# Kernel tuning notes

Measured on AMD Instinct MI355X. Metric: run time of the kernel, lower is better.

The kernel has to match this reference:

```python
import jax, jax.numpy as jnp
import numpy as np

B, T, K = 1024, 512, 48
NEG = -10000.0
START, STOP = K - 2, K - 1


def setup_inputs() -> dict:
    key = jax.random.key(0)
    k1, k2, k3 = jax.random.split(key, 3)
    feats = jax.random.normal(k1, (B, T, K), dtype=jnp.float32)
    transitions = jax.random.normal(k2, (K, K), dtype=jnp.float32) * 0.1
    tags = jax.random.randint(k3, (B, T), 0, K - 2)
    return {"feats": feats, "transitions": transitions, "tags": tags}


def _mask_trans(transitions):
    # transitions[next, prev]; never transition INTO START, never OUT of STOP
    t = transitions.at[START, :].set(NEG)
    t = t.at[:, STOP].set(NEG)
    return t


def _forward_alg(feats, trans):
    # feats: [T, K] -> log partition (scalar)
    Kt = feats.shape[-1]
    init = jnp.full((Kt,), NEG, dtype=feats.dtype).at[START].set(0.0)

    def step(alpha, emit):
        # alpha[prev] + trans[next, prev] -> LSE over prev, add emit[next]
        alpha_new = emit + jax.nn.logsumexp(alpha[None, :] + trans, axis=1)
        return alpha_new, None

    alpha, _ = jax.lax.scan(step, init, feats)
    return jax.nn.logsumexp(alpha + trans[STOP])


def _gold_score(feats, trans, tags):
    # feats: [T, K], tags: [T]
    Tt = tags.shape[0]
    prev = jnp.concatenate([jnp.array([START], dtype=tags.dtype), tags[:-1]])
    emit = feats[jnp.arange(Tt), tags].sum()
    tr = trans[tags, prev].sum()
    return emit + tr + trans[STOP, tags[-1]]


def _viterbi(feats, trans):
    Kt = feats.shape[-1]
    init = jnp.full((Kt,), NEG, dtype=feats.dtype).at[START].set(0.0)

    def step(v, emit):
        scores = v[None, :] + trans           # [next, prev]
        bp = jnp.argmax(scores, axis=1)       # best prev for each next
        v_new = jnp.max(scores, axis=1) + emit
        return v_new, bp

    v, bps = jax.lax.scan(step, init, feats)  # bps: [T, K]
    term = v + trans[STOP]
    best_last = jnp.argmax(term)
    path_score = term[best_last]

    def back(tag, bp):
        return bp[tag], tag

    _, path = jax.lax.scan(back, best_last, bps, reverse=True)
    return path_score, path.astype(jnp.int32)


def reference(feats, transitions, tags):
    trans = _mask_trans(transitions)
    logZ = jax.vmap(lambda f: _forward_alg(f, trans))(feats)            # [B]
    gold = jax.vmap(lambda f, t: _gold_score(f, trans, t))(feats, tags)  # [B]
    nll = logZ - gold                                                    # [B]
    path_score, paths = jax.vmap(lambda f: _viterbi(f, trans))(feats)    # [B], [B,T]
    return nll, path_score, paths
```

## Files before the change

### kernel.cpp

```cpp
#include <hip/hip_runtime.h>
#include <math.h>

#define KS 48
#define TLEN 512
#define BN 1024
#define START_S 46
#define STOP_S 47
#define NEGV -10000.0f
#define PF 8

typedef float v2f __attribute__((ext_vector_type(2)));

__device__ __forceinline__ float bcast_lane0(float v) {
    return __builtin_bit_cast(float, __builtin_amdgcn_readfirstlane(__builtin_bit_cast(int, v)));
}

__device__ __forceinline__ void wargmax(float& bv, int& bi) {
    #pragma unroll
    for (int off = 32; off; off >>= 1) {
        float ov = __shfl_xor(bv, off, 64);
        int   oi = __shfl_xor(bi, off, 64);
        if (ov > bv || (ov == bv && oi < bi)) { bv = ov; bi = oi; }
    }
}

__global__ __launch_bounds__(64) void crf11(
    const float* __restrict__ feats,
    const float* __restrict__ trans,
    const int*   __restrict__ tags,
    float*       __restrict__ out,
    unsigned char* __restrict__ bp_g)
{
    const int lane = threadIdx.x;
    const bool act = lane < KS;

    __shared__ float xbuf[64];
    __shared__ __align__(16) unsigned char seg[64 * KS];
    __shared__ unsigned char path_sh[TLEN];

    if (blockIdx.x < BN) {
        const int b = blockIdx.x;
        const float* fb = feats + (size_t)b * TLEN * KS;
        const int*   tb = tags + (size_t)b * TLEN;

        float Erow[KS];
        {
            const float* tr = trans + (act ? lane : 0) * KS;
            #pragma unroll
            for (int p = 0; p < KS; ++p) {
                float tv = act ? tr[p] : NEGV;
                if (lane == START_S) tv = NEGV;
                if (p == STOP_S)     tv = NEGV;
                Erow[p] = __expf(tv);
            }
        }
        float tstart = act ? trans[lane * KS + START_S] : NEGV;
        if (lane == START_S) tstart = NEGV;

        float alpha = (act ? fb[lane] : -INFINITY) + tstart;

        auto fstep = [&](float emv) {
            float s  = bcast_lane0(alpha);
            float ue = __expf(alpha - s);
            xbuf[lane] = ue;
            const float4* uu = (const float4*)xbuf;
            v2f acc0 = {0.f, 0.f}, acc1 = {0.f, 0.f};
            #pragma unroll
            for (int g = 0; g < KS / 4; ++g) {
                float4 u = uu[g];
                v2f ua = {u.x, u.y}, ub = {u.z, u.w};
                v2f ea = {Erow[4 * g + 0], Erow[4 * g + 1]};
                v2f eb = {Erow[4 * g + 2], Erow[4 * g + 3]};
                acc0 = __builtin_elementwise_fma(ua, ea, acc0);
                acc1 = __builtin_elementwise_fma(ub, eb, acc1);
            }
            alpha = emv + s + __logf((acc0.x + acc0.y) + (acc1.x + acc1.y));
        };

        float em[PF];
        #pragma unroll
        for (int j = 0; j < PF; ++j)
            em[j] = act ? fb[(1 + j) * KS + lane] : -INFINITY;
        for (int c = 0; c < 63; ++c) {
            const int t0 = 1 + c * PF;
            float em_n[PF];
            #pragma unroll
            for (int j = 0; j < PF; ++j) {
                int tf = t0 + PF + j;
                em_n[j] = (act && tf < TLEN) ? fb[tf * KS + lane] : -INFINITY;
            }
            #pragma unroll
            for (int j = 0; j < PF; ++j) fstep(em[j]);
            #pragma unroll
            for (int j = 0; j < PF; ++j) em[j] = em_n[j];
        }
        #pragma unroll
        for (int j = 0; j < 7; ++j) fstep(em[j]);

        float tstop = act ? trans[STOP_S * KS + lane] : NEGV;
        if (lane == STOP_S) tstop = NEGV;
        float z = alpha + tstop;
        float mz = z;
        #pragma unroll
        for (int off = 32; off; off >>= 1)
            mz = fmaxf(mz, __shfl_xor(mz, off, 64));
        float se = __expf(z - mz);
        #pragma unroll
        for (int off = 32; off; off >>= 1)
            se += __shfl_xor(se, off, 64);
        float logZ = mz + __logf(se);

        float g = 0.0f;
        for (int t = lane; t < TLEN; t += 64) {
            int tg = tb[t];
            int pg = (t == 0) ? START_S : tb[t - 1];
            g += fb[t * KS + tg] + trans[tg * KS + pg];
        }
        #pragma unroll
        for (int off = 32; off; off >>= 1)
            g += __shfl_xor(g, off, 64);
        g += trans[STOP_S * KS + tb[TLEN - 1]];

        if (lane == 0) out[b] = logZ - g;
    } else {
        const int b = blockIdx.x - BN;
        const float* fb = feats + (size_t)b * TLEN * KS;
        unsigned char* bpb = bp_g + (size_t)b * TLEN * KS;

        float Trow[KS];
        {
            const float* tr = trans + (act ? lane : 0) * KS;
            #pragma unroll
            for (int p = 0; p < KS; ++p) {
                float tv = act ? tr[p] : NEGV;
                if (lane == START_S) tv = NEGV;
                if (p == STOP_S)     tv = NEGV;
                Trow[p] = tv;
            }
        }

        float vit = (lane == START_S) ? 0.0f : NEGV;

        auto vstep = [&](float emv, int t) {
            xbuf[lane] = vit;
            const float4* ww = (const float4*)xbuf;
            float bs[12]; int ib[12];
            #pragma unroll
            for (int g = 0; g < KS / 4; ++g) {
                float4 w = ww[g];
                v2f wa = {w.x, w.y}, wb = {w.z, w.w};
                v2f ta = {Trow[4 * g + 0], Trow[4 * g + 1]};
                v2f tc = {Trow[4 * g + 2], Trow[4 * g + 3]};
                v2f sa = wa + ta;
                v2f sb = wb + tc;
                float m01 = fmaxf(sa.x, sa.y); int i01 = (sa.y > sa.x) ? 4 * g + 1 : 4 * g + 0;
                float m23 = fmaxf(sb.x, sb.y); int i23 = (sb.y > sb.x) ? 4 * g + 3 : 4 * g + 2;
                bs[g] = fmaxf(m01, m23);       ib[g] = (m23 > m01) ? i23 : i01;
            }
            #pragma unroll
            for (int st = 0; st < 6; ++st) {
                float a = bs[2 * st], c2 = bs[2 * st + 1];
                int ia = ib[2 * st], ic = ib[2 * st + 1];
                bs[st] = fmaxf(a, c2); ib[st] = (c2 > a) ? ic : ia;
            }
            #pragma unroll
            for (int st = 0; st < 3; ++st) {
                float a = bs[2 * st], c2 = bs[2 * st + 1];
                int ia = ib[2 * st], ic = ib[2 * st + 1];
                bs[st] = fmaxf(a, c2); ib[st] = (c2 > a) ? ic : ia;
            }
            float best = fmaxf(bs[0], bs[1]);
            int   bi   = (bs[1] > bs[0]) ? ib[1] : ib[0];
            bi   = (bs[2] > best) ? ib[2] : bi;
            best = fmaxf(best, bs[2]);
            if (act) seg[(t & 63) * KS + lane] = (unsigned char)bi;
            vit = best + emv;
        };

        float em[PF];
        #pragma unroll
        for (int j = 0; j < PF; ++j)
            em[j] = act ? fb[j * KS + lane] : 0.0f;
        for (int c = 0; c < 64; ++c) {
            const int t0 = c * PF;
            float em_n[PF];
            if (c < 63) {
                #pragma unroll
                for (int j = 0; j < PF; ++j)
                    em_n[j] = act ? fb[(t0 + PF + j) * KS + lane] : 0.0f;
            }
            #pragma unroll
            for (int j = 0; j < PF; ++j) vstep(em[j], t0 + j);
            if ((c & 7) == 7 && c < 56) {
                const float4* s4 = (const float4*)seg;
                float4* d4 = (float4*)(bpb + (size_t)(c - 7) * PF * KS);
                #pragma unroll
                for (int i = 0; i < 3; ++i)
                    d4[lane + 64 * i] = s4[lane + 64 * i];
            }
            if (c < 63) {
                #pragma unroll
                for (int j = 0; j < PF; ++j) em[j] = em_n[j];
            }
        }

        asm volatile("s_waitcnt vmcnt(0)" ::: "memory");

        float tstop = act ? trans[STOP_S * KS + lane] : NEGV;
        if (lane == STOP_S) tstop = NEGV;
        float term = act ? (vit + tstop) : -3.0e38f;
        float bv = term;
        int   bidx = act ? lane : 9999;
        wargmax(bv, bidx);
        if (lane == 0) out[BN + b] = bv;

        int tag = bidx;
        for (int t = 63; t >= 0; --t) {
            path_sh[448 + t] = (unsigned char)tag;
            tag = seg[t * KS + tag];
        }
        for (int s = 6; s >= 0; --s) {
            float4 tmp[3];
            const float4* src = (const float4*)(bpb + (size_t)s * 64 * KS);
            #pragma unroll
            for (int i = 0; i < 3; ++i)
                tmp[i] = src[lane + 64 * i];
            float4* dst = (float4*)seg;
            #pragma unroll
            for (int i = 0; i < 3; ++i)
                dst[lane + 64 * i] = tmp[i];
            for (int t = 63; t >= 0; --t) {
                path_sh[s * 64 + t] = (unsigned char)tag;
                tag = seg[t * KS + tag];
            }
        }
        __syncthreads();
        float* pout = out + 2 * BN + (size_t)b * TLEN;
        for (int t = lane; t < TLEN; t += 64)
            pout[t] = (float)path_sh[t];
    }
}

extern "C" void kernel_launch(void* const* d_in, const int* in_sizes, int n_in,
                              void* d_out, int out_size, void* d_ws, size_t ws_size,
                              hipStream_t stream) {
    const float* feats = (const float*)d_in[0];
    const float* trans = (const float*)d_in[1];
    const int*   tags  = (const int*)d_in[2];
    float*       out   = (float*)d_out;
    (void)in_sizes; (void)n_in; (void)out_size; (void)ws_size;

    crf11<<<dim3(2 * BN), dim3(64), 0, stream>>>(feats, trans, tags, out,
                                                 (unsigned char*)d_ws);
}
```

Baseline: 441.5 us.

## Fuse forward-algorithm and Viterbi recursions into one wave per sequence

Replaces the split launch (separate blocks for logZ and Viterbi per sequence) with a single block per sequence that interleaves the Viterbi step and the forward step at each time position. Emissions are loaded from global memory once and shared by both recursions, and the two independent dependency chains give the scheduler ILP to hide latency. The backpointer staging buffer is doubled to 128 rows so the last segment stays in LDS. In exchange each wave holds both Trow and Erow in registers (higher VGPR use), and only 1024 waves are launched instead of 2048, which lowers occupancy and parallelism across the GPU.

```diff
diff --git a/kernel.cpp b/kernel.cpp
--- a/kernel.cpp
+++ b/kernel.cpp
@@ -24,7 +24,7 @@
     }
 }
 
-__global__ __launch_bounds__(64) void crf11(
+__global__ __launch_bounds__(64) void crf13(
     const float* __restrict__ feats,
     const float* __restrict__ trans,
     const int*   __restrict__ tags,
@@ -34,71 +34,130 @@
     const int lane = threadIdx.x;
     const bool act = lane < KS;
 
-    __shared__ float xbuf[64];
-    __shared__ __align__(16) unsigned char seg[64 * KS];
+    __shared__ float xf[64];
+    __shared__ float xv[64];
+    __shared__ __align__(16) unsigned char seg[128 * KS];
     __shared__ unsigned char path_sh[TLEN];
 
-    if (blockIdx.x < BN) {
-        const int b = blockIdx.x;
-        const float* fb = feats + (size_t)b * TLEN * KS;
-        const int*   tb = tags + (size_t)b * TLEN;
-
-        float Erow[KS];
-        {
-            const float* tr = trans + (act ? lane : 0) * KS;
+    const int b = blockIdx.x;
+    const float* fb = feats + (size_t)b * TLEN * KS;
+    const int*   tb = tags + (size_t)b * TLEN;
+    unsigned char* bpb = bp_g + (size_t)b * TLEN * KS;
+
+    float Erow[KS], Trow[KS];
+    {
+        const float* tr = trans + (act ? lane : 0) * KS;
+        #pragma unroll
+        for (int p = 0; p < KS; ++p) {
+            float tv = act ? tr[p] : NEGV;
+            if (lane == START_S) tv = NEGV;
+            if (p == STOP_S)     tv = NEGV;
+            Trow[p] = tv;
+            Erow[p] = __expf(tv);
+        }
+    }
+    float tstart = act ? trans[lane * KS + START_S] : NEGV;
+    if (lane == START_S) tstart = NEGV;
+
+    float alpha;
+    auto fstep = [&](float emv) {
+        float s  = bcast_lane0(alpha);
+        float ue = __expf(alpha - s);
+        xf[lane] = ue;
+        const float4* uu = (const float4*)xf;
+        v2f acc0 = {0.f, 0.f}, acc1 = {0.f, 0.f};
+        #pragma unroll
+        for (int g = 0; g < KS / 4; ++g) {
+            float4 u = uu[g];
+            v2f ua = {u.x, u.y}, ub = {u.z, u.w};
+            v2f ea = {Erow[4 * g + 0], Erow[4 * g + 1]};
+            v2f eb = {Erow[4 * g + 2], Erow[4 * g + 3]};
+            acc0 = __builtin_elementwise_fma(ua, ea, acc0);
+            acc1 = __builtin_elementwise_fma(ub, eb, acc1);
+        }
+        alpha = emv + s + __logf((acc0.x + acc0.y) + (acc1.x + acc1.y));
+    };
+
+    float vit = (lane == START_S) ? 0.0f : NEGV;
+    auto vstep = [&](float emv, int t) {
+        xv[lane] = vit;
+        const float4* ww = (const float4*)xv;
+        float bs[12]; int ib[12];
+        #pragma unroll
+        for (int g = 0; g < KS / 4; ++g) {
+            float4 w = ww[g];
+            v2f wa = {w.x, w.y}, wb = {w.z, w.w};
+            v2f ta = {Trow[4 * g + 0], Trow[4 * g + 1]};
+            v2f tc = {Trow[4 * g + 2], Trow[4 * g + 3]};
+            v2f sa = wa + ta;
+            v2f sb = wb + tc;
+            float m01 = fmaxf(sa.x, sa.y); int i01 = (sa.y > sa.x) ? 4 * g + 1 : 4 * g + 0;
+            float m23 = fmaxf(sb.x, sb.y); int i23 = (sb.y > sb.x) ? 4 * g + 3 : 4 * g + 2;
+            bs[g] = fmaxf(m01, m23);       ib[g] = (m23 > m01) ? i23 : i01;
+        }
+        #pragma unroll
+        for (int st = 0; st < 6; ++st) {
+            float a = bs[2 * st], c2 = bs[2 * st + 1];
+            int ia = ib[2 * st], ic = ib[2 * st + 1];
+            bs[st] = fmaxf(a, c2); ib[st] = (c2 > a) ? ic : ia;
+        }
+        #pragma unroll
+        for (int st = 0; st < 3; ++st) {
+            float a = bs[2 * st], c2 = bs[2 * st + 1];
+            int ia = ib[2 * st], ic = ib[2 * st + 1];
+            bs[st] = fmaxf(a, c2); ib[st] = (c2 > a) ? ic : ia;
+        }
+        float best = fmaxf(bs[0], bs[1]);
+        int   bi   = (bs[1] > bs[0]) ? ib[1] : ib[0];
+        bi   = (bs[2] > best) ? ib[2] : bi;
+        best = fmaxf(best, bs[2]);
+        if (act) seg[(t & 127) * KS + lane] = (unsigned char)bi;
+        vit = best + emv;
+    };
+
+    float r0 = act ? fb[lane] : 0.0f;
+    alpha = (act ? r0 : -INFINITY) + tstart;
+    vstep(r0, 0);
+
+    float em[PF];
+    #pragma unroll
+    for (int j = 0; j < PF; ++j)
+        em[j] = act ? fb[(1 + j) * KS + lane] : 0.0f;
+    for (int c = 0; c < 63; ++c) {
+        const int t0 = 1 + c * PF;
+        float em_n[PF];
+        #pragma unroll
+        for (int j = 0; j < PF; ++j) {
+            int tf = t0 + PF + j;
+            em_n[j] = (act && tf < TLEN) ? fb[tf * KS + lane] : 0.0f;
+        }
+        #pragma unroll
+        for (int j = 0; j < PF; ++j) {
+            vstep(em[j], t0 + j);
+            fstep(em[j]);
+        }
+        if ((c & 7) == 7 && c < 56) {
+            const int g = c >> 3;
+            const float4* s4 = (const float4*)(seg + (g & 1) * 64 * KS);
+            float4* d4 = (float4*)(bpb + (size_t)g * 64 * KS);
             #pragma unroll
-            for (int p = 0; p < KS; ++p) {
-                float tv = act ? tr[p] : NEGV;
-                if (lane == START_S) tv = NEGV;
-                if (p == STOP_S)     tv = NEGV;
-                Erow[p] = __expf(tv);
-            }
-        }
-        float tstart = act ? trans[lane * KS + START_S] : NEGV;
-        if (lane == START_S) tstart = NEGV;
-
-        float alpha = (act ? fb[lane] : -INFINITY) + tstart;
-
-        auto fstep = [&](float emv) {
-            float s  = bcast_lane0(alpha);
-            float ue = __expf(alpha - s);
-            xbuf[lane] = ue;
-            const float4* uu = (const float4*)xbuf;
-            v2f acc0 = {0.f, 0.f}, acc1 = {0.f, 0.f};
-            #pragma unroll
-            for (int g = 0; g < KS / 4; ++g) {
-                float4 u = uu[g];
-                v2f ua = {u.x, u.y}, ub = {u.z, u.w};
-                v2f ea = {Erow[4 * g + 0], Erow[4 * g + 1]};
-                v2f eb = {Erow[4 * g + 2], Erow[4 * g + 3]};
-                acc0 = __builtin_elementwise_fma(ua, ea, acc0);
-                acc1 = __builtin_elementwise_fma(ub, eb, acc1);
-            }
-            alpha = emv + s + __logf((acc0.x + acc0.y) + (acc1.x + acc1.y));
-        };
-
-        float em[PF];
-        #pragma unroll
-        for (int j = 0; j < PF; ++j)
-            em[j] = act ? fb[(1 + j) * KS + lane] : -INFINITY;
-        for (int c = 0; c < 63; ++c) {
-            const int t0 = 1 + c * PF;
-            float em_n[PF];
-            #pragma unroll
-            for (int j = 0; j < PF; ++j) {
-                int tf = t0 + PF + j;
-                em_n[j] = (act && tf < TLEN) ? fb[tf * KS + lane] : -INFINITY;
-            }
-            #pragma unroll
-            for (int j = 0; j < PF; ++j) fstep(em[j]);
-            #pragma unroll
-            for (int j = 0; j < PF; ++j) em[j] = em_n[j];
-        }
-        #pragma unroll
-        for (int j = 0; j < 7; ++j) fstep(em[j]);
-
-        float tstop = act ? trans[STOP_S * KS + lane] : NEGV;
-        if (lane == STOP_S) tstop = NEGV;
+            for (int i = 0; i < 3; ++i)
+                d4[lane + 64 * i] = s4[lane + 64 * i];
+        }
+        #pragma unroll
+        for (int j = 0; j < PF; ++j) em[j] = em_n[j];
+    }
+    #pragma unroll
+    for (int j = 0; j < 7; ++j) {
+        vstep(em[j], 505 + j);
+        fstep(em[j]);
+    }
+
+    asm volatile("s_waitcnt vmcnt(0)" ::: "memory");
+
+    float tstop = act ? trans[STOP_S * KS + lane] : NEGV;
+    if (lane == STOP_S) tstop = NEGV;
+    {
         float z = alpha + tstop;
         float mz = z;
         #pragma unroll
@@ -122,123 +181,38 @@
         g += trans[STOP_S * KS + tb[TLEN - 1]];
 
         if (lane == 0) out[b] = logZ - g;
-    } else {
-        const int b = blockIdx.x - BN;
-        const float* fb = feats + (size_t)b * TLEN * KS;
-        unsigned char* bpb = bp_g + (size_t)b * TLEN * KS;
-
-        float Trow[KS];
-        {
-            const float* tr = trans + (act ? lane : 0) * KS;
-            #pragma unroll
-            for (int p = 0; p < KS; ++p) {
-                float tv = act ? tr[p] : NEGV;
-                if (lane == START_S) tv = NEGV;
-                if (p == STOP_S)     tv = NEGV;
-                Trow[p] = tv;
-            }
-        }
-
-        float vit = (lane == START_S) ? 0.0f : NEGV;
-
-        auto vstep = [&](float emv, int t) {
-            xbuf[lane] = vit;
-            const float4* ww = (const float4*)xbuf;
-            float bs[12]; int ib[12];
-            #pragma unroll
-            for (int g = 0; g < KS / 4; ++g) {
-                float4 w = ww[g];
-                v2f wa = {w.x, w.y}, wb = {w.z, w.w};
-                v2f ta = {Trow[4 * g + 0], Trow[4 * g + 1]};
-                v2f tc = {Trow[4 * g + 2], Trow[4 * g + 3]};
-                v2f sa = wa + ta;
-                v2f sb = wb + tc;
-                float m01 = fmaxf(sa.x, sa.y); int i01 = (sa.y > sa.x) ? 4 * g + 1 : 4 * g + 0;
-                float m23 = fmaxf(sb.x, sb.y); int i23 = (sb.y > sb.x) ? 4 * g + 3 : 4 * g + 2;
-                bs[g] = fmaxf(m01, m23);       ib[g] = (m23 > m01) ? i23 : i01;
-            }
-            #pragma unroll
-            for (int st = 0; st < 6; ++st) {
-                float a = bs[2 * st], c2 = bs[2 * st + 1];
-                int ia = ib[2 * st], ic = ib[2 * st + 1];
-                bs[st] = fmaxf(a, c2); ib[st] = (c2 > a) ? ic : ia;
-            }
-            #pragma unroll
-            for (int st = 0; st < 3; ++st) {
-                float a = bs[2 * st], c2 = bs[2 * st + 1];
-                int ia = ib[2 * st], ic = ib[2 * st + 1];
-                bs[st] = fmaxf(a, c2); ib[st] = (c2 > a) ? ic : ia;
-            }
-            float best = fmaxf(bs[0], bs[1]);
-            int   bi   = (bs[1] > bs[0]) ? ib[1] : ib[0];
-            bi   = (bs[2] > best) ? ib[2] : bi;
-            best = fmaxf(best, bs[2]);
-            if (act) seg[(t & 63) * KS + lane] = (unsigned char)bi;
-            vit = best + emv;
-        };
-
-        float em[PF];
-        #pragma unroll
-        for (int j = 0; j < PF; ++j)
-            em[j] = act ? fb[j * KS + lane] : 0.0f;
-        for (int c = 0; c < 64; ++c) {
-            const int t0 = c * PF;
-            float em_n[PF];
-            if (c < 63) {
-                #pragma unroll
-                for (int j = 0; j < PF; ++j)
-                    em_n[j] = act ? fb[(t0 + PF + j) * KS + lane] : 0.0f;
-            }
-            #pragma unroll
-            for (int j = 0; j < PF; ++j) vstep(em[j], t0 + j);
-            if ((c & 7) == 7 && c < 56) {
-                const float4* s4 = (const float4*)seg;
-                float4* d4 = (float4*)(bpb + (size_t)(c - 7) * PF * KS);
-                #pragma unroll
-                for (int i = 0; i < 3; ++i)
-                    d4[lane + 64 * i] = s4[lane + 64 * i];
-            }
-            if (c < 63) {
-                #pragma unroll
-                for (int j = 0; j < PF; ++j) em[j] = em_n[j];
-            }
-        }
-
-        asm volatile("s_waitcnt vmcnt(0)" ::: "memory");
-
-        float tstop = act ? trans[STOP_S * KS + lane] : NEGV;
-        if (lane == STOP_S) tstop = NEGV;
-        float term = act ? (vit + tstop) : -3.0e38f;
-        float bv = term;
-        int   bidx = act ? lane : 9999;
-        wargmax(bv, bidx);
-        if (lane == 0) out[BN + b] = bv;
-
-        int tag = bidx;
+    }
+
+    float term = act ? (vit + tstop) : -3.0e38f;
+    float bv = term;
+    int   bidx = act ? lane : 9999;
+    wargmax(bv, bidx);
+    if (lane == 0) out[BN + b] = bv;
+
+    int tag = bidx;
+    for (int t = 63; t >= 0; --t) {
+        path_sh[448 + t] = (unsigned char)tag;
+        tag = seg[(64 + t) * KS + tag];
+    }
+    for (int s = 6; s >= 0; --s) {
+        float4 tmp[3];
+        const float4* src = (const float4*)(bpb + (size_t)s * 64 * KS);
+        #pragma unroll
+        for (int i = 0; i < 3; ++i)
+            tmp[i] = src[lane + 64 * i];
+        float4* dst = (float4*)seg;
+        #pragma unroll
+        for (int i = 0; i < 3; ++i)
+            dst[lane + 64 * i] = tmp[i];
         for (int t = 63; t >= 0; --t) {
-            path_sh[448 + t] = (unsigned char)tag;
+            path_sh[s * 64 + t] = (unsigned char)tag;
             tag = seg[t * KS + tag];
         }
-        for (int s = 6; s >= 0; --s) {
-            float4 tmp[3];
-            const float4* src = (const float4*)(bpb + (size_t)s * 64 * KS);
-            #pragma unroll
-            for (int i = 0; i < 3; ++i)
-                tmp[i] = src[lane + 64 * i];
-            float4* dst = (float4*)seg;
-            #pragma unroll
-            for (int i = 0; i < 3; ++i)
-                dst[lane + 64 * i] = tmp[i];
-            for (int t = 63; t >= 0; --t) {
-                path_sh[s * 64 + t] = (unsigned char)tag;
-                tag = seg[t * KS + tag];
-            }
-        }
-        __syncthreads();
-        float* pout = out + 2 * BN + (size_t)b * TLEN;
-        for (int t = lane; t < TLEN; t += 64)
-            pout[t] = (float)path_sh[t];
-    }
+    }
+    __syncthreads();
+    float* pout = out + 2 * BN + (size_t)b * TLEN;
+    for (int t = lane; t < TLEN; t += 64)
+        pout[t] = (float)path_sh[t];
 }
 
 extern "C" void kernel_launch(void* const* d_in, const int* in_sizes, int n_in,
@@ -250,6 +224,6 @@
     float*       out   = (float*)d_out;
     (void)in_sizes; (void)n_in; (void)out_size; (void)ws_size;
 
-    crf11<<<dim3(2 * BN), dim3(64), 0, stream>>>(feats, trans, tags, out,
-                                                 (unsigned char*)d_ws);
-}
+    crf13<<<dim3(BN), dim3(64), 0, stream>>>(feats, trans, tags, out,
+                                             (unsigned char*)d_ws);
+}
```

New measurement: 530.7 us. +20.2%, slower.

## Split fused CRF kernel into forward, Viterbi scan, and backtrace kernels

Applied to the files above, without the earlier changes.

Replaces the single 2048-block kernel, which branched between forward-algorithm and Viterbi work, with three back-to-back launches: forward/NLL, Viterbi scan that writes all backpointers and the final tag to workspace, and a separate backtrace kernel. The aim is to shorten the Viterbi critical path by moving the serial backtrace into its own launch and to give each kernel lower register and LDS use. The costs are serialized launches, since the forward and Viterbi work no longer run concurrently in one grid, plus an extra global round trip for the last backpointer segment.

```diff
diff --git a/kernel.cpp b/kernel.cpp
--- a/kernel.cpp
+++ b/kernel.cpp
@@ -24,221 +24,241 @@
     }
 }
 
-__global__ __launch_bounds__(64) void crf11(
-    const float* __restrict__ feats,
-    const float* __restrict__ trans,
-    const int*   __restrict__ tags,
-    float*       __restrict__ out,
-    unsigned char* __restrict__ bp_g)
+
+__global__ __launch_bounds__(64) void crf_fwd(
+    const float* __restrict__ feats, const float* __restrict__ trans,
+    const int* __restrict__ tags, float* __restrict__ out)
 {
     const int lane = threadIdx.x;
     const bool act = lane < KS;
-
+    __shared__ float xbuf[64];
+
+    const int b = blockIdx.x;
+    const float* fb = feats + (size_t)b * TLEN * KS;
+    const int*   tb = tags + (size_t)b * TLEN;
+
+    float Erow[KS];
+    {
+        const float* tr = trans + (act ? lane : 0) * KS;
+        #pragma unroll
+        for (int p = 0; p < KS; ++p) {
+            float tv = act ? tr[p] : NEGV;
+            if (lane == START_S) tv = NEGV;
+            if (p == STOP_S)     tv = NEGV;
+            Erow[p] = __expf(tv);
+        }
+    }
+    float tstart = act ? trans[lane * KS + START_S] : NEGV;
+    if (lane == START_S) tstart = NEGV;
+
+    float alpha = (act ? fb[lane] : -INFINITY) + tstart;
+
+    auto fstep = [&](float emv) {
+        float s  = bcast_lane0(alpha);
+        float ue = __expf(alpha - s);
+        xbuf[lane] = ue;
+        const float4* uu = (const float4*)xbuf;
+        v2f acc0 = {0.f, 0.f}, acc1 = {0.f, 0.f};
+        #pragma unroll
+        for (int g = 0; g < KS / 4; ++g) {
+            float4 u = uu[g];
+            v2f ua = {u.x, u.y}, ub = {u.z, u.w};
+            v2f ea = {Erow[4 * g + 0], Erow[4 * g + 1]};
+            v2f eb = {Erow[4 * g + 2], Erow[4 * g + 3]};
+            acc0 = __builtin_elementwise_fma(ua, ea, acc0);
+            acc1 = __builtin_elementwise_fma(ub, eb, acc1);
+        }
+        alpha = emv + s + __logf((acc0.x + acc0.y) + (acc1.x + acc1.y));
+    };
+
+    float em[PF];
+    #pragma unroll
+    for (int j = 0; j < PF; ++j)
+        em[j] = act ? fb[(1 + j) * KS + lane] : -INFINITY;
+    for (int c = 0; c < 63; ++c) {
+        const int t0 = 1 + c * PF;
+        float em_n[PF];
+        #pragma unroll
+        for (int j = 0; j < PF; ++j) {
+            int tf = t0 + PF + j;
+            em_n[j] = (act && tf < TLEN) ? fb[tf * KS + lane] : -INFINITY;
+        }
+        #pragma unroll
+        for (int j = 0; j < PF; ++j) fstep(em[j]);
+        #pragma unroll
+        for (int j = 0; j < PF; ++j) em[j] = em_n[j];
+    }
+    #pragma unroll
+    for (int j = 0; j < 7; ++j) fstep(em[j]);
+
+    float tstop = act ? trans[STOP_S * KS + lane] : NEGV;
+    if (lane == STOP_S) tstop = NEGV;
+    float z = alpha + tstop;
+    float mz = z;
+    #pragma unroll
+    for (int off = 32; off; off >>= 1)
+        mz = fmaxf(mz, __shfl_xor(mz, off, 64));
+    float se = __expf(z - mz);
+    #pragma unroll
+    for (int off = 32; off; off >>= 1)
+        se += __shfl_xor(se, off, 64);
+    float logZ = mz + __logf(se);
+
+    float g = 0.0f;
+    for (int t = lane; t < TLEN; t += 64) {
+        int tg = tb[t];
+        int pg = (t == 0) ? START_S : tb[t - 1];
+        g += fb[t * KS + tg] + trans[tg * KS + pg];
+    }
+    #pragma unroll
+    for (int off = 32; off; off >>= 1)
+        g += __shfl_xor(g, off, 64);
+    g += trans[STOP_S * KS + tb[TLEN - 1]];
+
+    if (lane == 0) out[b] = logZ - g;
+}
+
+__global__ __launch_bounds__(64) void crf_vit_scan(
+    const float* __restrict__ feats, const float* __restrict__ trans,
+    float* __restrict__ out, unsigned char* __restrict__ bp_g,
+    int* __restrict__ tag0_g)
+{
+    const int lane = threadIdx.x;
+    const bool act = lane < KS;
     __shared__ float xbuf[64];
     __shared__ __align__(16) unsigned char seg[64 * KS];
-    __shared__ unsigned char path_sh[TLEN];
-
-    if (blockIdx.x < BN) {
-        const int b = blockIdx.x;
-        const float* fb = feats + (size_t)b * TLEN * KS;
-        const int*   tb = tags + (size_t)b * TLEN;
-
-        float Erow[KS];
-        {
-            const float* tr = trans + (act ? lane : 0) * KS;
+
+    const int b = blockIdx.x;
+    const float* fb = feats + (size_t)b * TLEN * KS;
+    unsigned char* bpb = bp_g + (size_t)b * TLEN * KS;
+
+    float Trow[KS];
+    {
+        const float* tr = trans + (act ? lane : 0) * KS;
+        #pragma unroll
+        for (int p = 0; p < KS; ++p) {
+            float tv = act ? tr[p] : NEGV;
+            if (lane == START_S) tv = NEGV;
+            if (p == STOP_S)     tv = NEGV;
+            Trow[p] = tv;
+        }
+    }
+
+    float vit = (lane == START_S) ? 0.0f : NEGV;
+
+    auto vstep = [&](float emv, int t) {
+        xbuf[lane] = vit;
+        const float4* ww = (const float4*)xbuf;
+        float bs[12]; int ib[12];
+        #pragma unroll
+        for (int g = 0; g < KS / 4; ++g) {
+            float4 w = ww[g];
+            v2f wa = {w.x, w.y}, wb = {w.z, w.w};
+            v2f ta = {Trow[4 * g + 0], Trow[4 * g + 1]};
+            v2f tc = {Trow[4 * g + 2], Trow[4 * g + 3]};
+            v2f sa = wa + ta;
+            v2f sb = wb + tc;
+            float m01 = fmaxf(sa.x, sa.y); int i01 = (sa.y > sa.x) ? 4 * g + 1 : 4 * g + 0;
+            float m23 = fmaxf(sb.x, sb.y); int i23 = (sb.y > sb.x) ? 4 * g + 3 : 4 * g + 2;
+            bs[g] = fmaxf(m01, m23);       ib[g] = (m23 > m01) ? i23 : i01;
+        }
+        #pragma unroll
+        for (int st = 0; st < 6; ++st) {
+            float a = bs[2 * st], c2 = bs[2 * st + 1];
+            int ia = ib[2 * st], ic = ib[2 * st + 1];
+            bs[st] = fmaxf(a, c2); ib[st] = (c2 > a) ? ic : ia;
+        }
+        #pragma unroll
+        for (int st = 0; st < 3; ++st) {
+            float a = bs[2 * st], c2 = bs[2 * st + 1];
+            int ia = ib[2 * st], ic = ib[2 * st + 1];
+            bs[st] = fmaxf(a, c2); ib[st] = (c2 > a) ? ic : ia;
+        }
+        float best = fmaxf(bs[0], bs[1]);
+        int   bi   = (bs[1] > bs[0]) ? ib[1] : ib[0];
+        bi   = (bs[2] > best) ? ib[2] : bi;
+        best = fmaxf(best, bs[2]);
+        if (act) seg[(t & 63) * KS + lane] = (unsigned char)bi;
+        vit = best + emv;
+    };
+
+    float em[PF];
+    #pragma unroll
+    for (int j = 0; j < PF; ++j)
+        em[j] = act ? fb[j * KS + lane] : 0.0f;
+    for (int c = 0; c < 64; ++c) {
+        const int t0 = c * PF;
+        float em_n[PF];
+        if (c < 63) {
             #pragma unroll
-            for (int p = 0; p < KS; ++p) {
-                float tv = act ? tr[p] : NEGV;
-                if (lane == START_S) tv = NEGV;
-                if (p == STOP_S)     tv = NEGV;
-                Erow[p] = __expf(tv);
-            }
-        }
-        float tstart = act ? trans[lane * KS + START_S] : NEGV;
-        if (lane == START_S) tstart = NEGV;
-
-        float alpha = (act ? fb[lane] : -INFINITY) + tstart;
-
-        auto fstep = [&](float emv) {
-            float s  = bcast_lane0(alpha);
-            float ue = __expf(alpha - s);
-            xbuf[lane] = ue;
-            const float4* uu = (const float4*)xbuf;
-            v2f acc0 = {0.f, 0.f}, acc1 = {0.f, 0.f};
+            for (int j = 0; j < PF; ++j)
+                em_n[j] = act ? fb[(t0 + PF + j) * KS + lane] : 0.0f;
+        }
+        #pragma unroll
+        for (int j = 0; j < PF; ++j) vstep(em[j], t0 + j);
+        if ((c & 7) == 7 && c < 56) {
+            const float4* s4 = (const float4*)seg;
+            float4* d4 = (float4*)(bpb + (size_t)(c - 7) * PF * KS);
             #pragma unroll
-            for (int g = 0; g < KS / 4; ++g) {
-                float4 u = uu[g];
-                v2f ua = {u.x, u.y}, ub = {u.z, u.w};
-                v2f ea = {Erow[4 * g + 0], Erow[4 * g + 1]};
-                v2f eb = {Erow[4 * g + 2], Erow[4 * g + 3]};
-                acc0 = __builtin_elementwise_fma(ua, ea, acc0);
-                acc1 = __builtin_elementwise_fma(ub, eb, acc1);
-            }
-            alpha = emv + s + __logf((acc0.x + acc0.y) + (acc1.x + acc1.y));
-        };
-
-        float em[PF];
-        #pragma unroll
-        for (int j = 0; j < PF; ++j)
-            em[j] = act ? fb[(1 + j) * KS + lane] : -INFINITY;
-        for (int c = 0; c < 63; ++c) {
-            const int t0 = 1 + c * PF;
-            float em_n[PF];
-            #pragma unroll
-            for (int j = 0; j < PF; ++j) {
-                int tf = t0 + PF + j;
-                em_n[j] = (act && tf < TLEN) ? fb[tf * KS + lane] : -INFINITY;
-            }
-            #pragma unroll
-            for (int j = 0; j < PF; ++j) fstep(em[j]);
+            for (int i = 0; i < 3; ++i)
+                d4[lane + 64 * i] = s4[lane + 64 * i];
+        }
+        if (c < 63) {
             #pragma unroll
             for (int j = 0; j < PF; ++j) em[j] = em_n[j];
         }
-        #pragma unroll
-        for (int j = 0; j < 7; ++j) fstep(em[j]);
-
-        float tstop = act ? trans[STOP_S * KS + lane] : NEGV;
-        if (lane == STOP_S) tstop = NEGV;
-        float z = alpha + tstop;
-        float mz = z;
-        #pragma unroll
-        for (int off = 32; off; off >>= 1)
-            mz = fmaxf(mz, __shfl_xor(mz, off, 64));
-        float se = __expf(z - mz);
-        #pragma unroll
-        for (int off = 32; off; off >>= 1)
-            se += __shfl_xor(se, off, 64);
-        float logZ = mz + __logf(se);
-
-        float g = 0.0f;
-        for (int t = lane; t < TLEN; t += 64) {
-            int tg = tb[t];
-            int pg = (t == 0) ? START_S : tb[t - 1];
-            g += fb[t * KS + tg] + trans[tg * KS + pg];
-        }
-        #pragma unroll
-        for (int off = 32; off; off >>= 1)
-            g += __shfl_xor(g, off, 64);
-        g += trans[STOP_S * KS + tb[TLEN - 1]];
-
-        if (lane == 0) out[b] = logZ - g;
-    } else {
-        const int b = blockIdx.x - BN;
-        const float* fb = feats + (size_t)b * TLEN * KS;
-        unsigned char* bpb = bp_g + (size_t)b * TLEN * KS;
-
-        float Trow[KS];
-        {
-            const float* tr = trans + (act ? lane : 0) * KS;
-            #pragma unroll
-            for (int p = 0; p < KS; ++p) {
-                float tv = act ? tr[p] : NEGV;
-                if (lane == START_S) tv = NEGV;
-                if (p == STOP_S)     tv = NEGV;
-                Trow[p] = tv;
-            }
-        }
-
-        float vit = (lane == START_S) ? 0.0f : NEGV;
-
-        auto vstep = [&](float emv, int t) {
-            xbuf[lane] = vit;
-            const float4* ww = (const float4*)xbuf;
-            float bs[12]; int ib[12];
-            #pragma unroll
-            for (int g = 0; g < KS / 4; ++g) {
-                float4 w = ww[g];
-                v2f wa = {w.x, w.y}, wb = {w.z, w.w};
-                v2f ta = {Trow[4 * g + 0], Trow[4 * g + 1]};
-                v2f tc = {Trow[4 * g + 2], Trow[4 * g + 3]};
-                v2f sa = wa + ta;
-                v2f sb = wb + tc;
-                float m01 = fmaxf(sa.x, sa.y); int i01 = (sa.y > sa.x) ? 4 * g + 1 : 4 * g + 0;
-                float m23 = fmaxf(sb.x, sb.y); int i23 = (sb.y > sb.x) ? 4 * g + 3 : 4 * g + 2;
-                bs[g] = fmaxf(m01, m23);       ib[g] = (m23 > m01) ? i23 : i01;
-            }
-            #pragma unroll
-            for (int st = 0; st < 6; ++st) {
-                float a = bs[2 * st], c2 = bs[2 * st + 1];
-                int ia = ib[2 * st], ic = ib[2 * st + 1];
-                bs[st] = fmaxf(a, c2); ib[st] = (c2 > a) ? ic : ia;
-            }
-            #pragma unroll
-            for (int st = 0; st < 3; ++st) {
-                float a = bs[2 * st], c2 = bs[2 * st + 1];
-                int ia = ib[2 * st], ic = ib[2 * st + 1];
-                bs[st] = fmaxf(a, c2); ib[st] = (c2 > a) ? ic : ia;
-            }
-            float best = fmaxf(bs[0], bs[1]);
-            int   bi   = (bs[1] > bs[0]) ? ib[1] : ib[0];
-            bi   = (bs[2] > best) ? ib[2] : bi;
-            best = fmaxf(best, bs[2]);
-            if (act) seg[(t & 63) * KS + lane] = (unsigned char)bi;
-            vit = best + emv;
-        };
-
-        float em[PF];
-        #pragma unroll
-        for (int j = 0; j < PF; ++j)
-            em[j] = act ? fb[j * KS + lane] : 0.0f;
-        for (int c = 0; c < 64; ++c) {
-            const int t0 = c * PF;
-            float em_n[PF];
-            if (c < 63) {
-                #pragma unroll
-                for (int j = 0; j < PF; ++j)
-                    em_n[j] = act ? fb[(t0 + PF + j) * KS + lane] : 0.0f;
-            }
-            #pragma unroll
-            for (int j = 0; j < PF; ++j) vstep(em[j], t0 + j);
-            if ((c & 7) == 7 && c < 56) {
-                const float4* s4 = (const float4*)seg;
-                float4* d4 = (float4*)(bpb + (size_t)(c - 7) * PF * KS);
-                #pragma unroll
-                for (int i = 0; i < 3; ++i)
-                    d4[lane + 64 * i] = s4[lane + 64 * i];
-            }
-            if (c < 63) {
-                #pragma unroll
-                for (int j = 0; j < PF; ++j) em[j] = em_n[j];
-            }
-        }
-
-        asm volatile("s_waitcnt vmcnt(0)" ::: "memory");
-
-        float tstop = act ? trans[STOP_S * KS + lane] : NEGV;
-        if (lane == STOP_S) tstop = NEGV;
-        float term = act ? (vit + tstop) : -3.0e38f;
-        float bv = term;
-        int   bidx = act ? lane : 9999;
-        wargmax(bv, bidx);
-        if (lane == 0) out[BN + b] = bv;
-
-        int tag = bidx;
+    }
+    {
+        const float4* s4 = (const float4*)seg;
+        float4* d4 = (float4*)(bpb + (size_t)7 * 64 * KS);
+        #pragma unroll
+        for (int i = 0; i < 3; ++i)
+            d4[lane + 64 * i] = s4[lane + 64 * i];
+    }
+
+    float tstop = act ? trans[STOP_S * KS + lane] : NEGV;
+    if (lane == STOP_S) tstop = NEGV;
+    float term = act ? (vit + tstop) : -3.0e38f;
+    float bv = term;
+    int   bidx = act ? lane : 9999;
+    wargmax(bv, bidx);
+    if (lane == 0) {
+        out[BN + b] = bv;
+        tag0_g[b] = bidx;
+    }
+}
+
+__global__ __launch_bounds__(64) void crf_bt(
+    const unsigned char* __restrict__ bp_g, const int* __restrict__ tag0_g,
+    float* __restrict__ out)
+{
+    const int lane = threadIdx.x;
+    __shared__ __align__(16) unsigned char seg[64 * KS];
+    __shared__ unsigned char path_sh[TLEN];
+
+    const int b = blockIdx.x;
+    const unsigned char* bpb = bp_g + (size_t)b * TLEN * KS;
+
+    int tag = tag0_g[b];
+    for (int s = 7; s >= 0; --s) {
+        float4 tmp[3];
+        const float4* src = (const float4*)(bpb + (size_t)s * 64 * KS);
+        #pragma unroll
+        for (int i = 0; i < 3; ++i)
+            tmp[i] = src[lane + 64 * i];
+        float4* dst = (float4*)seg;
+        #pragma unroll
+        for (int i = 0; i < 3; ++i)
+            dst[lane + 64 * i] = tmp[i];
         for (int t = 63; t >= 0; --t) {
-            path_sh[448 + t] = (unsigned char)tag;
+            path_sh[s * 64 + t] = (unsigned char)tag;
             tag = seg[t * KS + tag];
         }
-        for (int s = 6; s >= 0; --s) {
-            float4 tmp[3];
-            const float4* src = (const float4*)(bpb + (size_t)s * 64 * KS);
-            #pragma unroll
-            for (int i = 0; i < 3; ++i)
-                tmp[i] = src[lane + 64 * i];
-            float4* dst = (float4*)seg;
-            #pragma unroll
-            for (int i = 0; i < 3; ++i)
-                dst[lane + 64 * i] = tmp[i];
-            for (int t = 63; t >= 0; --t) {
-                path_sh[s * 64 + t] = (unsigned char)tag;
-                tag = seg[t * KS + tag];
-            }
-        }
-        __syncthreads();
-        float* pout = out + 2 * BN + (size_t)b * TLEN;
-        for (int t = lane; t < TLEN; t += 64)
-            pout[t] = (float)path_sh[t];
-    }
+    }
+    __syncthreads();
+    float* pout = out + 2 * BN + (size_t)b * TLEN;
+    for (int t = lane; t < TLEN; t += 64)
+        pout[t] = (float)path_sh[t];
 }
 
 extern "C" void kernel_launch(void* const* d_in, const int* in_sizes, int n_in,
@@ -250,6 +270,10 @@
     float*       out   = (float*)d_out;
     (void)in_sizes; (void)n_in; (void)out_size; (void)ws_size;
 
-    crf11<<<dim3(2 * BN), dim3(64), 0, stream>>>(feats, trans, tags, out,
-                                                 (unsigned char*)d_ws);
-}
+    unsigned char* bp = (unsigned char*)d_ws;
+    int* tag0 = (int*)((unsigned char*)d_ws + (size_t)BN * TLEN * KS);
+
+    crf_fwd<<<dim3(BN), dim3(64), 0, stream>>>(feats, trans, tags, out);
+    crf_vit_scan<<<dim3(BN), dim3(64), 0, stream>>>(feats, trans, out, bp, tag0);
+    crf_bt<<<dim3(BN), dim3(64), 0, stream>>>(bp, tag0, out);
+}
```

New measurement: 550.1 us. 24.6% more time.
